# Optimization experiments

Measured on AMD Instinct MI355X. Metric: run time of the kernel, lower is better.

The kernel has to match this reference:

```python
import jax, jax.numpy as jnp
import numpy as np

LN_EPS = 1e-5  # torch.nn.LayerNorm default

def g(x):
    # minGRU activation: x + 0.5 for x >= 0, sigmoid(x) otherwise (always positive)
    return jnp.where(x >= 0, x + 0.5, jax.nn.sigmoid(x))

def log_g(x):
    return jnp.where(x >= 0, jnp.log(jax.nn.relu(x) + 0.5), -jax.nn.softplus(-x))

def layernorm(x, gamma, beta):
    mu = jnp.mean(x, axis=-1, keepdims=True)
    var = jnp.var(x, axis=-1, keepdims=True)
    return (x - mu) * jax.lax.rsqrt(var + LN_EPS) * gamma + beta

def mingru_scan(gate, hidden, h0):
    # gate, hidden: (B,S,D); h0: (B,1,D) positive
    # z = sigmoid(gate); h_t = (1-z_t)*h_{t-1} + z_t * g(hidden_t)
    # evaluated via Heinsen parallel scan in log space
    log_z = -jax.nn.softplus(-gate)          # log sigmoid(gate)
    log_coeffs = -jax.nn.softplus(gate)      # log(1 - sigmoid(gate))
    log_h0 = jnp.log(h0)                     # (B,1,D)
    log_tilde_h = log_g(hidden)
    a_star = jnp.cumsum(
        jnp.concatenate([jnp.zeros_like(log_h0), log_coeffs], axis=1), axis=1
    )                                        # (B,S+1,D)
    log_vals = jnp.concatenate([log_h0, log_z + log_tilde_h], axis=1) - a_star
    log_h = a_star + jax.lax.cumlogsumexp(log_vals, axis=1)
    return jnp.exp(log_h)[:, 1:]             # (B,S,D)

def setup_inputs() -> dict:
    key = jax.random.key(0)
    k1, k2 = jax.random.split(key)
    B, S, D, L = 8, 4096, 1024, 3
    x = jax.random.normal(k1, (B, S, D), dtype=jnp.float32)
    W = jax.random.normal(k2, (L, D, 2 * D), dtype=jnp.float32) * 0.02
    b = jnp.zeros((L, 2 * D), dtype=jnp.float32)
    ln_gamma = jnp.ones((L, D), dtype=jnp.float32)
    ln_beta = jnp.zeros((L, D), dtype=jnp.float32)
    return {"x": x, "ln_gamma": ln_gamma, "ln_beta": ln_beta, "W": W, "b": b}

def reference(x, ln_gamma, ln_beta, W, b):
    B, S, D = x.shape
    L = W.shape[0]
    inp = x
    next_hidden = []
    for l in range(L):
        h_prev = jnp.full((B, 1, D), 0.5, dtype=x.dtype)  # g(zeros) = 0.5
        xn = layernorm(inp, ln_gamma[l], ln_beta[l])
        gh = jnp.einsum('bsd,de->bse', xn, W[l]) + b[l]   # (B,S,2D)
        gate, hidden = jnp.split(gh, 2, axis=2)
        out = mingru_scan(gate, hidden, h_prev)
        next_hidden.append(out[:, -1:])
        out = out + inp  # residual (sizes equal -> identity res_align)
        inp = out
    return (out, *next_hidden)
```

## Files before the change

### kernel.cpp

```cpp
#include <hip/hip_runtime.h>

typedef unsigned short u16;
typedef unsigned int   u32;
typedef float  f32x4  __attribute__((ext_vector_type(4)));
typedef short  bf16x8 __attribute__((ext_vector_type(8)));
typedef u16    u16x4  __attribute__((ext_vector_type(4)));

#define BQ 8
#define SQ 4096
#define DQ 1024
#define NQ 2048
#define MQ 32768
#define KQ 1024
#define CCH 64
#define TCH 64
#define NT 16

__device__ __forceinline__ float bf2f(u16 u){
  union { u32 i; float f; } v; v.i = ((u32)u) << 16; return v.f;
}
__device__ __forceinline__ u16 f2bf(float f){
  union { float f; u32 i; } v; v.f = f;
  u32 r = v.i + 0x7fffu + ((v.i >> 16) & 1u);
  return (u16)(r >> 16);
}

__device__ __forceinline__ void sig_ab(float gate, float hid, float& a, float& bv){
  float eg = __expf(gate);
  float a_ = __builtin_amdgcn_rcpf(1.f + eg);
  float z  = 1.f - a_;
  float eh = __expf(hid);
  float sg = eh * __builtin_amdgcn_rcpf(1.f + eh);
  float gval = (hid >= 0.f) ? (hid + 0.5f) : sg;
  a = a_; bv = z * gval;
}

__device__ __forceinline__ void gload_lds16(const u16* g, u16* l){
  __builtin_amdgcn_global_load_lds(
      (const __attribute__((address_space(1))) u32*)g,
      (__attribute__((address_space(3)))       u32*)l,
      16, 0, 0);
}

__global__ __launch_bounds__(256) void wt_cast(const float* __restrict__ W,
                                               u16* __restrict__ WT){
  __shared__ float t[64][65];
  const int l  = blockIdx.z;
  const int k0 = blockIdx.x << 6, n0 = blockIdx.y << 6;
  const float* Wl = W  + (size_t)l * KQ * NQ;
  u16*         Tl = WT + (size_t)l * NQ * KQ;
  const int c = threadIdx.x & 63, r4 = threadIdx.x >> 6;
  #pragma unroll
  for (int i = 0; i < 16; ++i){
    int r = i * 4 + r4;
    t[r][c] = Wl[(size_t)(k0 + r) * NQ + n0 + c];
  }
  __syncthreads();
  #pragma unroll
  for (int i = 0; i < 16; ++i){
    int r = i * 4 + r4;
    Tl[(size_t)(n0 + r) * KQ + k0 + c] = f2bf(t[c][r]);
  }
}

__global__ __launch_bounds__(256) void ln_cast(const float* __restrict__ x,
                                               const float* __restrict__ gamma,
                                               const float* __restrict__ beta,
                                               u16* __restrict__ xn){
  const size_t row = blockIdx.x;
  const int tid = threadIdx.x;
  f32x4 xv = *(const f32x4*)(x + row * DQ + tid * 4);
  float s  = xv[0] + xv[1] + xv[2] + xv[3];
  float s2 = xv[0]*xv[0] + xv[1]*xv[1] + xv[2]*xv[2] + xv[3]*xv[3];
  #pragma unroll
  for (int off = 32; off > 0; off >>= 1){
    s  += __shfl_down(s,  off);
    s2 += __shfl_down(s2, off);
  }
  __shared__ float red[8];
  const int wave = tid >> 6, lane = tid & 63;
  if (lane == 0){ red[wave] = s; red[4 + wave] = s2; }
  __syncthreads();
  s  = red[0] + red[1] + red[2] + red[3];
  s2 = red[4] + red[5] + red[6] + red[7];
  const float mean = s * (1.f / DQ);
  float var = fmaxf(s2 * (1.f / DQ) - mean * mean, 0.f);
  const float rstd = rsqrtf(var + 1e-5f);
  f32x4 gv = *(const f32x4*)(gamma + tid * 4);
  f32x4 bv = *(const f32x4*)(beta  + tid * 4);
  u16x4 o;
  #pragma unroll
  for (int e = 0; e < 4; ++e) o[e] = f2bf((xv[e] - mean) * rstd * gv[e] + bv[e]);
  *(u16x4*)(xn + row * DQ + tid * 4) = o;
}

__global__ __launch_bounds__(512, 2) void gemm_k8(const u16* __restrict__ A,
                                                  const u16* __restrict__ Bt,
                                                  const float* __restrict__ bias,
                                                  u16* __restrict__ Cg){
  __shared__ u16 lds[2][2][2][8192];
  const int bid = blockIdx.x;
  const int swz = ((bid & 7) << 7) | (bid >> 3);
  const int bn = swz & 7, bm = swz >> 3;
  const int n0 = bn << 8, m0 = bm << 8;
  const int tid = threadIdx.x;
  const int w = tid >> 6, lane = tid & 63;
  const int wr = w >> 2, wc = w & 3;
  const int lr = lane & 15, hi = lane >> 4;
  const int sl8 = lane >> 3;
  const int sslot = (lane & 7) ^ sl8;

  f32x4 acc[2][2][4][2] = {};
  bf16x8 afr[4][2];
  bf16x8 bf0[2][2], bf1[2][2];

#define FENCE asm volatile("" ::: "memory")
#define BAR do { FENCE; __builtin_amdgcn_s_barrier(); FENCE; } while(0)

#define STAGE(op, hf, kt, pb_) do {                                             \
    const u16* gsrc_ = (op) ? Bt : A;                                           \
    const int rb_ = ((op) ? n0 : m0) + ((hf) << 7);                             \
    _Pragma("unroll")                                                           \
    for (int g_ = 0; g_ < 2; ++g_){                                             \
      const int row_ = (w << 4) + (g_ << 3) + sl8;                              \
      gload_lds16(gsrc_ + (size_t)(rb_ + row_) * KQ + ((kt) << 6) + (sslot << 3),\
                  &lds[pb_][op][hf][((w << 4) + (g_ << 3)) << 6]);              \
    }                                                                           \
  } while(0)

#define LDSRD(dst, base_, row_, slot_) do {                                     \
    const int r_ = (row_);                                                      \
    dst = *(const bf16x8*)((const char*)(base_) +                               \
          ((r_ << 7) + ((((slot_)) ^ (r_ & 7)) << 4)));                         \
  } while(0)

#define RD_A(hf) do {                                                           \
    const u16* Ah_ = &lds[pb][0][hf][0];                                        \
    _Pragma("unroll")                                                           \
    for (int i_ = 0; i_ < 4; ++i_)                                              \
      _Pragma("unroll")                                                         \
      for (int kk_ = 0; kk_ < 2; ++kk_)                                         \
        LDSRD(afr[i_][kk_], Ah_, (wr << 6) + (i_ << 4) + lr, (kk_ << 2) + hi);  \
  } while(0)

#define RD_B(dst, hf) do {                                                      \
    const u16* Bh_ = &lds[pb][1][hf][0];                                        \
    _Pragma("unroll")                                                           \
    for (int j_ = 0; j_ < 2; ++j_)                                              \
      _Pragma("unroll")                                                         \
      for (int kk_ = 0; kk_ < 2; ++kk_)                                         \
        LDSRD(dst[j_][kk_], Bh_, (wc << 5) + (j_ << 4) + lr, (kk_ << 2) + hi);  \
  } while(0)

#define MM(qm, qn, B) do {                                                      \
    _Pragma("unroll")                                                           \
    for (int i_ = 0; i_ < 4; ++i_)                                              \
      _Pragma("unroll")                                                         \
      for (int j_ = 0; j_ < 2; ++j_)                                            \
        _Pragma("unroll")                                                       \
        for (int kk_ = 0; kk_ < 2; ++kk_)                                       \
          acc[qm][qn][i_][j_] = __builtin_amdgcn_mfma_f32_16x16x32_bf16(        \
              afr[i_][kk_], B[j_][kk_], acc[qm][qn][i_][j_], 0, 0, 0);          \
  } while(0)

#define PH(VMW, STG, RDS, MFMAS) do {                                           \
    VMW;                                                                        \
    BAR;                                                                        \
    STG;                                                                        \
    RDS;                                                                        \
    asm volatile("s_waitcnt lgkmcnt(0)" ::: "memory");                          \
    __builtin_amdgcn_s_setprio(1);                                              \
    MFMAS;                                                                      \
    __builtin_amdgcn_s_setprio(0);                                              \
  } while(0)

  STAGE(1, 0, 0, 0); STAGE(0, 0, 0, 0); STAGE(1, 1, 0, 0); STAGE(0, 1, 0, 0);

  for (int t = 0; t < NT; ++t){
    const int pb = t & 1, qb = pb ^ 1;
    const bool s = (t + 1 < NT);
    PH(asm volatile("s_waitcnt vmcnt(4)" ::: "memory"),
       if (s) STAGE(1, 0, t + 1, qb),
       RD_A(0); RD_B(bf0, 0),
       MM(0, 0, bf0));
    PH(if (s) { asm volatile("s_waitcnt vmcnt(4)" ::: "memory"); }
       else   { asm volatile("s_waitcnt vmcnt(2)" ::: "memory"); },
       if (s) STAGE(0, 0, t + 1, qb),
       RD_B(bf1, 1),
       MM(0, 1, bf1));
    PH(if (s) { asm volatile("s_waitcnt vmcnt(4)" ::: "memory"); }
       else   { asm volatile("s_waitcnt vmcnt(0)" ::: "memory"); },
       if (s) STAGE(1, 1, t + 1, qb),
       RD_A(1),
       MM(1, 0, bf0));
    PH(,
       if (s) STAGE(0, 1, t + 1, qb),
       ,
       MM(1, 1, bf1));
  }
#undef PH
#undef MM
#undef RD_B
#undef RD_A
#undef LDSRD
#undef STAGE

  #pragma unroll
  for (int qn = 0; qn < 2; ++qn)
    #pragma unroll
    for (int j = 0; j < 2; ++j){
      const int col = n0 + (qn << 7) + (wc << 5) + (j << 4) + lr;
      const float bj = bias[col];
      #pragma unroll
      for (int qm = 0; qm < 2; ++qm)
        #pragma unroll
        for (int i = 0; i < 4; ++i){
          const int row0 = m0 + (qm << 7) + (wr << 6) + (i << 4) + (hi << 2);
          #pragma unroll
          for (int r = 0; r < 4; ++r)
            Cg[(size_t)(row0 + r) * NQ + col] = f2bf(acc[qm][qn][i][j][r] + bj);
        }
    }
#undef BAR
#undef FENCE
}

__global__ __launch_bounds__(256) void scan1(const u16* __restrict__ gh,
                                             float* __restrict__ P,
                                             float* __restrict__ Q){
  const int b = blockIdx.x >> 6;
  const int c = blockIdx.x & 63;
  const int d4 = threadIdx.x << 2;
  const u16* base = gh + ((size_t)(b * SQ + c * TCH) * NQ) + d4;
  float p[4] = {1.f,1.f,1.f,1.f}, q[4] = {0.f,0.f,0.f,0.f};
  for (int t = 0; t < TCH; ++t){
    u16x4 gv = *(const u16x4*)(base + (size_t)t * NQ);
    u16x4 hv = *(const u16x4*)(base + (size_t)t * NQ + DQ);
    #pragma unroll
    for (int e = 0; e < 4; ++e){
      float a, bv; sig_ab(bf2f(gv[e]), bf2f(hv[e]), a, bv);
      p[e] *= a; q[e] = a * q[e] + bv;
    }
  }
  const size_t o = ((size_t)blockIdx.x << 10) + d4;
  *(f32x4*)(P + o) = f32x4{p[0], p[1], p[2], p[3]};
  *(f32x4*)(Q + o) = f32x4{q[0], q[1], q[2], q[3]};
}

__global__ __launch_bounds__(256) void scan2(const float* __restrict__ P,
                                             const float* __restrict__ Q,
                                             float* __restrict__ hst,
                                             float* __restrict__ hlast){
  const int idx = blockIdx.x * 256 + threadIdx.x;
  const int b = idx >> 10, d = idx & 1023;
  float h = 0.5f;
  for (int c = 0; c < CCH; ++c){
    const size_t o = ((size_t)(b * CCH + c) << 10) + d;
    hst[o] = h;
    h = P[o] * h + Q[o];
  }
  hlast[idx] = h;
}

template<int MODE>
__global__ __launch_bounds__(256) void scan3f(const u16* __restrict__ gh,
                                              const float* __restrict__ hst,
                                              const void* __restrict__ inp,
                                              void* __restrict__ outp,
                                              u16* __restrict__ xn,
                                              const float* __restrict__ gamma,
                                              const float* __restrict__ beta){
  const int b = blockIdx.x >> 6;
  const int c = blockIdx.x & 63;
  const int tid = threadIdx.x;
  const int d4 = tid << 2;
  const int wave = tid >> 6, lane = tid & 63;
  const size_t srow = (size_t)(b * SQ + c * TCH);
  const u16* base = gh + srow * NQ + d4;
  const size_t o = ((size_t)blockIdx.x << 10) + d4;
  f32x4 h0v = *(const f32x4*)(hst + o);
  float h[4] = {h0v[0], h0v[1], h0v[2], h0v[3]};
  __shared__ float red[2][8];
  f32x4 gv = {}, bvv = {};
  if (MODE != 2){
    gv  = *(const f32x4*)(gamma + d4);
    bvv = *(const f32x4*)(beta  + d4);
  }
  for (int t = 0; t < TCH; ++t){
    u16x4 gg = *(const u16x4*)(base + (size_t)t * NQ);
    u16x4 hh = *(const u16x4*)(base + (size_t)t * NQ + DQ);
    f32x4 iv;
    if (MODE == 0){
      iv = *(const f32x4*)((const float*)inp + (srow + t) * DQ + d4);
    } else {
      u16x4 ib = *(const u16x4*)((const u16*)inp + (srow + t) * DQ + d4);
      #pragma unroll
      for (int e = 0; e < 4; ++e) iv[e] = bf2f(ib[e]);
    }
    f32x4 ov;
    #pragma unroll
    for (int e = 0; e < 4; ++e){
      float a, bv; sig_ab(bf2f(gg[e]), bf2f(hh[e]), a, bv);
      h[e] = a * h[e] + bv;
      ov[e] = h[e] + iv[e];
    }
    if (MODE == 2){
      *(f32x4*)((float*)outp + (srow + t) * DQ + d4) = ov;
    } else {
      u16x4 ob;
      #pragma unroll
      for (int e = 0; e < 4; ++e) ob[e] = f2bf(ov[e]);
      *(u16x4*)((u16*)outp + (srow + t) * DQ + d4) = ob;
      float s  = ov[0] + ov[1] + ov[2] + ov[3];
      float s2 = ov[0]*ov[0] + ov[1]*ov[1] + ov[2]*ov[2] + ov[3]*ov[3];
      #pragma unroll
      for (int off = 32; off > 0; off >>= 1){
        s  += __shfl_down(s,  off);
        s2 += __shfl_down(s2, off);
      }
      const int rb = t & 1;
      if (lane == 0){ red[rb][wave] = s; red[rb][4 + wave] = s2; }
      __syncthreads();
      s  = red[rb][0] + red[rb][1] + red[rb][2] + red[rb][3];
      s2 = red[rb][4] + red[rb][5] + red[rb][6] + red[rb][7];
      const float mean = s * (1.f / DQ);
      float var = fmaxf(s2 * (1.f / DQ) - mean * mean, 0.f);
      const float rstd = rsqrtf(var + 1e-5f);
      u16x4 xo;
      #pragma unroll
      for (int e = 0; e < 4; ++e)
        xo[e] = f2bf((ov[e] - mean) * rstd * gv[e] + bvv[e]);
      *(u16x4*)(xn + (srow + t) * DQ + d4) = xo;
    }
  }
}

extern "C" void kernel_launch(void* const* d_in, const int* in_sizes, int n_in,
                              void* d_out, int out_size, void* d_ws, size_t ws_size,
                              hipStream_t stream) {
  const float* x     = (const float*)d_in[0];
  const float* gamma = (const float*)d_in[1];
  const float* beta  = (const float*)d_in[2];
  const float* W     = (const float*)d_in[3];
  const float* bias  = (const float*)d_in[4];
  float* out = (float*)d_out;

  char* ws = (char*)d_ws;
  const size_t ACT = (size_t)MQ * DQ * 4;
  u16*   bufA = (u16*)(ws);
  u16*   bufB = (u16*)(ws + ACT);
  u16*   gh   = (u16*)  (ws + 2 * ACT);
  u16*   xn   = (u16*)  (ws + 3 * ACT);
  u16*   WT   = (u16*)  (ws + 3 * ACT + (size_t)MQ * DQ * 2);
  float* Pa   = (float*)(ws + 3 * ACT + (size_t)MQ * DQ * 2 + (size_t)3 * NQ * KQ * 2);
  float* Qa   = Pa + (size_t)BQ * CCH * DQ;
  float* hst  = Qa + (size_t)BQ * CCH * DQ;

  wt_cast<<<dim3(KQ / 64, NQ / 64, 3), 256, 0, stream>>>(W, WT);

  ln_cast<<<MQ, 256, 0, stream>>>(x, gamma, beta, xn);
  gemm_k8<<<dim3((NQ / 256) * (MQ / 256)), 512, 0, stream>>>(xn, WT, bias, gh);
  scan1<<<BQ * CCH, 256, 0, stream>>>(gh, Pa, Qa);
  scan2<<<(BQ * DQ) / 256, 256, 0, stream>>>(Pa, Qa, hst, out + (size_t)MQ * DQ);
  scan3f<0><<<BQ * CCH, 256, 0, stream>>>(gh, hst, x, bufA, xn,
                                          gamma + DQ, beta + DQ);
  gemm_k8<<<dim3((NQ / 256) * (MQ / 256)), 512, 0, stream>>>(
      xn, WT + (size_t)NQ * KQ, bias + NQ, gh);
  scan1<<<BQ * CCH, 256, 0, stream>>>(gh, Pa, Qa);
  scan2<<<(BQ * DQ) / 256, 256, 0, stream>>>(Pa, Qa, hst,
                                             out + (size_t)MQ * DQ + BQ * DQ);
  scan3f<1><<<BQ * CCH, 256, 0, stream>>>(gh, hst, bufA, bufB, xn,
                                          gamma + 2 * DQ, beta + 2 * DQ);
  gemm_k8<<<dim3((NQ / 256) * (MQ / 256)), 512, 0, stream>>>(
      xn, WT + (size_t)2 * NQ * KQ, bias + 2 * NQ, gh);
  scan1<<<BQ * CCH, 256, 0, stream>>>(gh, Pa, Qa);
  scan2<<<(BQ * DQ) / 256, 256, 0, stream>>>(Pa, Qa, hst,
                                             out + (size_t)MQ * DQ + 2 * BQ * DQ);
  scan3f<2><<<BQ * CCH, 256, 0, stream>>>(gh, hst, bufB, out, nullptr,
                                          nullptr, nullptr);
}
```

Measured before the change: 814.5 us.

## Fuse sigmoid coefficients and chunk scan summaries into the GEMM epilogue

The GEMM tiling changes so each block's N tile holds matching gate and hidden columns (128 of each). The epilogue then computes the recurrence coefficients a and b, stores them packed as bf16 pairs, and reduces per-64-row chunk (P,Q) summaries with cross-lane shuffles. This removes the scan1 kernel and its full re-read of the gate/hidden tensor, and scan3f no longer recomputes the sigmoids. The cost is a heavier GEMM epilogue with scattered 4-byte stores and a changed (P,Q) layout.

```diff
diff --git a/kernel.cpp b/kernel.cpp
--- a/kernel.cpp
+++ b/kernel.cpp
@@ -2,9 +2,11 @@
 
 typedef unsigned short u16;
 typedef unsigned int   u32;
+typedef float  f32x2  __attribute__((ext_vector_type(2)));
 typedef float  f32x4  __attribute__((ext_vector_type(4)));
 typedef short  bf16x8 __attribute__((ext_vector_type(8)));
 typedef u16    u16x4  __attribute__((ext_vector_type(4)));
+typedef u32    u32x4  __attribute__((ext_vector_type(4)));
 
 #define BQ 8
 #define SQ 4096
@@ -97,12 +99,13 @@
 __global__ __launch_bounds__(512, 2) void gemm_k8(const u16* __restrict__ A,
                                                   const u16* __restrict__ Bt,
                                                   const float* __restrict__ bias,
-                                                  u16* __restrict__ Cg){
+                                                  u32* __restrict__ abv,
+                                                  float* __restrict__ pq){
   __shared__ u16 lds[2][2][2][8192];
   const int bid = blockIdx.x;
   const int swz = ((bid & 7) << 7) | (bid >> 3);
   const int bn = swz & 7, bm = swz >> 3;
-  const int n0 = bn << 8, m0 = bm << 8;
+  const int m0 = bm << 8;
   const int tid = threadIdx.x;
   const int w = tid >> 6, lane = tid & 63;
   const int wr = w >> 2, wc = w & 3;
@@ -117,61 +120,61 @@
 #define FENCE asm volatile("" ::: "memory")
 #define BAR do { FENCE; __builtin_amdgcn_s_barrier(); FENCE; } while(0)
 
-#define STAGE(op, hf, kt, pb_) do {                                             \
-    const u16* gsrc_ = (op) ? Bt : A;                                           \
-    const int rb_ = ((op) ? n0 : m0) + ((hf) << 7);                             \
-    _Pragma("unroll")                                                           \
-    for (int g_ = 0; g_ < 2; ++g_){                                             \
-      const int row_ = (w << 4) + (g_ << 3) + sl8;                              \
+#define STAGE(op, hf, kt, pb_) do {                                            \
+    const u16* gsrc_ = (op) ? Bt : A;                                          \
+    const int rb_ = (op) ? ((bn << 7) + (hf) * 1024) : (m0 + ((hf) << 7));     \
+    _Pragma("unroll")                                                          \
+    for (int g_ = 0; g_ < 2; ++g_){                                            \
+      const int row_ = (w << 4) + (g_ << 3) + sl8;                             \
       gload_lds16(gsrc_ + (size_t)(rb_ + row_) * KQ + ((kt) << 6) + (sslot << 3),\
-                  &lds[pb_][op][hf][((w << 4) + (g_ << 3)) << 6]);              \
-    }                                                                           \
-  } while(0)
-
-#define LDSRD(dst, base_, row_, slot_) do {                                     \
-    const int r_ = (row_);                                                      \
-    dst = *(const bf16x8*)((const char*)(base_) +                               \
-          ((r_ << 7) + ((((slot_)) ^ (r_ & 7)) << 4)));                         \
-  } while(0)
-
-#define RD_A(hf) do {                                                           \
-    const u16* Ah_ = &lds[pb][0][hf][0];                                        \
-    _Pragma("unroll")                                                           \
-    for (int i_ = 0; i_ < 4; ++i_)                                              \
-      _Pragma("unroll")                                                         \
-      for (int kk_ = 0; kk_ < 2; ++kk_)                                         \
-        LDSRD(afr[i_][kk_], Ah_, (wr << 6) + (i_ << 4) + lr, (kk_ << 2) + hi);  \
-  } while(0)
-
-#define RD_B(dst, hf) do {                                                      \
-    const u16* Bh_ = &lds[pb][1][hf][0];                                        \
-    _Pragma("unroll")                                                           \
-    for (int j_ = 0; j_ < 2; ++j_)                                              \
-      _Pragma("unroll")                                                         \
-      for (int kk_ = 0; kk_ < 2; ++kk_)                                         \
-        LDSRD(dst[j_][kk_], Bh_, (wc << 5) + (j_ << 4) + lr, (kk_ << 2) + hi);  \
-  } while(0)
-
-#define MM(qm, qn, B) do {                                                      \
-    _Pragma("unroll")                                                           \
-    for (int i_ = 0; i_ < 4; ++i_)                                              \
-      _Pragma("unroll")                                                         \
-      for (int j_ = 0; j_ < 2; ++j_)                                            \
-        _Pragma("unroll")                                                       \
-        for (int kk_ = 0; kk_ < 2; ++kk_)                                       \
-          acc[qm][qn][i_][j_] = __builtin_amdgcn_mfma_f32_16x16x32_bf16(        \
-              afr[i_][kk_], B[j_][kk_], acc[qm][qn][i_][j_], 0, 0, 0);          \
-  } while(0)
-
-#define PH(VMW, STG, RDS, MFMAS) do {                                           \
-    VMW;                                                                        \
-    BAR;                                                                        \
-    STG;                                                                        \
-    RDS;                                                                        \
-    asm volatile("s_waitcnt lgkmcnt(0)" ::: "memory");                          \
-    __builtin_amdgcn_s_setprio(1);                                              \
-    MFMAS;                                                                      \
-    __builtin_amdgcn_s_setprio(0);                                              \
+                  &lds[pb_][op][hf][((w << 4) + (g_ << 3)) << 6]);             \
+    }                                                                          \
+  } while(0)
+
+#define LDSRD(dst, base_, row_, slot_) do {                                    \
+    const int r_ = (row_);                                                     \
+    dst = *(const bf16x8*)((const char*)(base_) +                              \
+          ((r_ << 7) + ((((slot_)) ^ (r_ & 7)) << 4)));                        \
+  } while(0)
+
+#define RD_A(hf) do {                                                          \
+    const u16* Ah_ = &lds[pb][0][hf][0];                                       \
+    _Pragma("unroll")                                                          \
+    for (int i_ = 0; i_ < 4; ++i_)                                             \
+      _Pragma("unroll")                                                        \
+      for (int kk_ = 0; kk_ < 2; ++kk_)                                        \
+        LDSRD(afr[i_][kk_], Ah_, (wr << 6) + (i_ << 4) + lr, (kk_ << 2) + hi); \
+  } while(0)
+
+#define RD_B(dst, hf) do {                                                     \
+    const u16* Bh_ = &lds[pb][1][hf][0];                                       \
+    _Pragma("unroll")                                                          \
+    for (int j_ = 0; j_ < 2; ++j_)                                             \
+      _Pragma("unroll")                                                        \
+      for (int kk_ = 0; kk_ < 2; ++kk_)                                        \
+        LDSRD(dst[j_][kk_], Bh_, (wc << 5) + (j_ << 4) + lr, (kk_ << 2) + hi); \
+  } while(0)
+
+#define MM(qm, qn, B) do {                                                     \
+    _Pragma("unroll")                                                          \
+    for (int i_ = 0; i_ < 4; ++i_)                                             \
+      _Pragma("unroll")                                                        \
+      for (int j_ = 0; j_ < 2; ++j_)                                           \
+        _Pragma("unroll")                                                      \
+        for (int kk_ = 0; kk_ < 2; ++kk_)                                      \
+          acc[qm][qn][i_][j_] = __builtin_amdgcn_mfma_f32_16x16x32_bf16(       \
+              afr[i_][kk_], B[j_][kk_], acc[qm][qn][i_][j_], 0, 0, 0);         \
+  } while(0)
+
+#define PH(VMW, STG, RDS, MFMAS) do {                                          \
+    VMW;                                                                       \
+    BAR;                                                                       \
+    STG;                                                                       \
+    RDS;                                                                       \
+    asm volatile("s_waitcnt lgkmcnt(0)" ::: "memory");                         \
+    __builtin_amdgcn_s_setprio(1);                                             \
+    MFMAS;                                                                     \
+    __builtin_amdgcn_s_setprio(0);                                             \
   } while(0)
 
   STAGE(1, 0, 0, 0); STAGE(0, 0, 0, 0); STAGE(1, 1, 0, 0); STAGE(0, 1, 0, 0);
@@ -205,50 +208,56 @@
 #undef LDSRD
 #undef STAGE
 
-  #pragma unroll
-  for (int qn = 0; qn < 2; ++qn)
+  const int dbase = (bn << 7) + (wc << 5) + lr;
+  #pragma unroll
+  for (int qm = 0; qm < 2; ++qm){
+    const int row00 = m0 + (qm << 7) + (wr << 6);
+    float chP[2] = {1.f, 1.f}, chQ[2] = {0.f, 0.f};
     #pragma unroll
-    for (int j = 0; j < 2; ++j){
-      const int col = n0 + (qn << 7) + (wc << 5) + (j << 4) + lr;
-      const float bj = bias[col];
-      #pragma unroll
-      for (int qm = 0; qm < 2; ++qm)
+    for (int i = 0; i < 4; ++i){
+      float sgP[2] = {1.f, 1.f}, sgQ[2] = {0.f, 0.f};
+      #pragma unroll
+      for (int r = 0; r < 4; ++r){
+        const int row = row00 + (i << 4) + (hi << 2) + r;
         #pragma unroll
-        for (int i = 0; i < 4; ++i){
-          const int row0 = m0 + (qm << 7) + (wr << 6) + (i << 4) + (hi << 2);
-          #pragma unroll
-          for (int r = 0; r < 4; ++r)
-            Cg[(size_t)(row0 + r) * NQ + col] = f2bf(acc[qm][qn][i][j][r] + bj);
+        for (int j = 0; j < 2; ++j){
+          const int d = dbase + (j << 4);
+          float gate = acc[qm][0][i][j][r] + bias[d];
+          float hid  = acc[qm][1][i][j][r] + bias[1024 + d];
+          float a, bv; sig_ab(gate, hid, a, bv);
+          const u16 ua = f2bf(a), ub = f2bf(bv);
+          abv[(size_t)row * 1024 + d] = (u32)ua | ((u32)ub << 16);
+          const float ar = bf2f(ua), br = bf2f(ub);
+          sgQ[j] = ar * sgQ[j] + br;
+          sgP[j] *= ar;
         }
-    }
+      }
+      #pragma unroll
+      for (int j = 0; j < 2; ++j){
+        float p = sgP[j], q = sgQ[j];
+        float p1 = __shfl_up(p, 16), q1 = __shfl_up(q, 16);
+        if (hi >= 1){ q = p * q1 + q; p = p * p1; }
+        float p2 = __shfl_up(p, 32), q2 = __shfl_up(q, 32);
+        if (hi >= 2){ q = p * q2 + q; p = p * p2; }
+        chQ[j] = p * chQ[j] + q;
+        chP[j] = p * chP[j];
+      }
+    }
+    if (hi == 3){
+      const int bq = row00 >> 12, cq = (row00 >> 6) & 63;
+      #pragma unroll
+      for (int j = 0; j < 2; ++j){
+        const int d = dbase + (j << 4);
+        f32x2 v; v[0] = chP[j]; v[1] = chQ[j];
+        *(f32x2*)(pq + ((((size_t)(bq * CCH + cq)) << 10) + d) * 2) = v;
+      }
+    }
+  }
 #undef BAR
 #undef FENCE
 }
 
-__global__ __launch_bounds__(256) void scan1(const u16* __restrict__ gh,
-                                             float* __restrict__ P,
-                                             float* __restrict__ Q){
-  const int b = blockIdx.x >> 6;
-  const int c = blockIdx.x & 63;
-  const int d4 = threadIdx.x << 2;
-  const u16* base = gh + ((size_t)(b * SQ + c * TCH) * NQ) + d4;
-  float p[4] = {1.f,1.f,1.f,1.f}, q[4] = {0.f,0.f,0.f,0.f};
-  for (int t = 0; t < TCH; ++t){
-    u16x4 gv = *(const u16x4*)(base + (size_t)t * NQ);
-    u16x4 hv = *(const u16x4*)(base + (size_t)t * NQ + DQ);
-    #pragma unroll
-    for (int e = 0; e < 4; ++e){
-      float a, bv; sig_ab(bf2f(gv[e]), bf2f(hv[e]), a, bv);
-      p[e] *= a; q[e] = a * q[e] + bv;
-    }
-  }
-  const size_t o = ((size_t)blockIdx.x << 10) + d4;
-  *(f32x4*)(P + o) = f32x4{p[0], p[1], p[2], p[3]};
-  *(f32x4*)(Q + o) = f32x4{q[0], q[1], q[2], q[3]};
-}
-
-__global__ __launch_bounds__(256) void scan2(const float* __restrict__ P,
-                                             const float* __restrict__ Q,
+__global__ __launch_bounds__(256) void scan2(const float* __restrict__ pq,
                                              float* __restrict__ hst,
                                              float* __restrict__ hlast){
   const int idx = blockIdx.x * 256 + threadIdx.x;
@@ -257,13 +266,14 @@
   for (int c = 0; c < CCH; ++c){
     const size_t o = ((size_t)(b * CCH + c) << 10) + d;
     hst[o] = h;
-    h = P[o] * h + Q[o];
+    f32x2 v = *(const f32x2*)(pq + o * 2);
+    h = v[0] * h + v[1];
   }
   hlast[idx] = h;
 }
 
 template<int MODE>
-__global__ __launch_bounds__(256) void scan3f(const u16* __restrict__ gh,
+__global__ __launch_bounds__(256) void scan3f(const u32* __restrict__ abv,
                                               const float* __restrict__ hst,
                                               const void* __restrict__ inp,
                                               void* __restrict__ outp,
@@ -276,7 +286,7 @@
   const int d4 = tid << 2;
   const int wave = tid >> 6, lane = tid & 63;
   const size_t srow = (size_t)(b * SQ + c * TCH);
-  const u16* base = gh + srow * NQ + d4;
+  const u32* base = abv + srow * 1024 + d4;
   const size_t o = ((size_t)blockIdx.x << 10) + d4;
   f32x4 h0v = *(const f32x4*)(hst + o);
   float h[4] = {h0v[0], h0v[1], h0v[2], h0v[3]};
@@ -287,8 +297,7 @@
     bvv = *(const f32x4*)(beta  + d4);
   }
   for (int t = 0; t < TCH; ++t){
-    u16x4 gg = *(const u16x4*)(base + (size_t)t * NQ);
-    u16x4 hh = *(const u16x4*)(base + (size_t)t * NQ + DQ);
+    u32x4 ab = *(const u32x4*)(base + (size_t)t * 1024);
     f32x4 iv;
     if (MODE == 0){
       iv = *(const f32x4*)((const float*)inp + (srow + t) * DQ + d4);
@@ -300,7 +309,8 @@
     f32x4 ov;
     #pragma unroll
     for (int e = 0; e < 4; ++e){
-      float a, bv; sig_ab(bf2f(gg[e]), bf2f(hh[e]), a, bv);
+      const float a  = bf2f((u16)(ab[e] & 0xffffu));
+      const float bv = bf2f((u16)(ab[e] >> 16));
       h[e] = a * h[e] + bv;
       ov[e] = h[e] + iv[e];
     }
@@ -349,33 +359,30 @@
   const size_t ACT = (size_t)MQ * DQ * 4;
   u16*   bufA = (u16*)(ws);
   u16*   bufB = (u16*)(ws + ACT);
-  u16*   gh   = (u16*)  (ws + 2 * ACT);
-  u16*   xn   = (u16*)  (ws + 3 * ACT);
-  u16*   WT   = (u16*)  (ws + 3 * ACT + (size_t)MQ * DQ * 2);
-  float* Pa   = (float*)(ws + 3 * ACT + (size_t)MQ * DQ * 2 + (size_t)3 * NQ * KQ * 2);
-  float* Qa   = Pa + (size_t)BQ * CCH * DQ;
-  float* hst  = Qa + (size_t)BQ * CCH * DQ;
+  u32*   abv  = (u32*)(ws + 2 * ACT);
+  u16*   xn   = (u16*)(ws + 3 * ACT);
+  u16*   WT   = (u16*)(ws + 3 * ACT + (size_t)MQ * DQ * 2);
+  float* pq   = (float*)(ws + 3 * ACT + (size_t)MQ * DQ * 2 + (size_t)3 * NQ * KQ * 2);
+  float* hst  = pq + (size_t)2 * BQ * CCH * DQ;
 
   wt_cast<<<dim3(KQ / 64, NQ / 64, 3), 256, 0, stream>>>(W, WT);
 
+  const dim3 ggrid((NQ / 256) * (MQ / 256));
   ln_cast<<<MQ, 256, 0, stream>>>(x, gamma, beta, xn);
-  gemm_k8<<<dim3((NQ / 256) * (MQ / 256)), 512, 0, stream>>>(xn, WT, bias, gh);
-  scan1<<<BQ * CCH, 256, 0, stream>>>(gh, Pa, Qa);
-  scan2<<<(BQ * DQ) / 256, 256, 0, stream>>>(Pa, Qa, hst, out + (size_t)MQ * DQ);
-  scan3f<0><<<BQ * CCH, 256, 0, stream>>>(gh, hst, x, bufA, xn,
+  gemm_k8<<<ggrid, 512, 0, stream>>>(xn, WT, bias, abv, pq);
+  scan2<<<(BQ * DQ) / 256, 256, 0, stream>>>(pq, hst, out + (size_t)MQ * DQ);
+  scan3f<0><<<BQ * CCH, 256, 0, stream>>>(abv, hst, x, bufA, xn,
                                           gamma + DQ, beta + DQ);
-  gemm_k8<<<dim3((NQ / 256) * (MQ / 256)), 512, 0, stream>>>(
-      xn, WT + (size_t)NQ * KQ, bias + NQ, gh);
-  scan1<<<BQ * CCH, 256, 0, stream>>>(gh, Pa, Qa);
-  scan2<<<(BQ * DQ) / 256, 256, 0, stream>>>(Pa, Qa, hst,
+  gemm_k8<<<ggrid, 512, 0, stream>>>(xn, WT + (size_t)NQ * KQ, bias + NQ,
+                                     abv, pq);
+  scan2<<<(BQ * DQ) / 256, 256, 0, stream>>>(pq, hst,
                                              out + (size_t)MQ * DQ + BQ * DQ);
-  scan3f<1><<<BQ * CCH, 256, 0, stream>>>(gh, hst, bufA, bufB, xn,
+  scan3f<1><<<BQ * CCH, 256, 0, stream>>>(abv, hst, bufA, bufB, xn,
                                           gamma + 2 * DQ, beta + 2 * DQ);
-  gemm_k8<<<dim3((NQ / 256) * (MQ / 256)), 512, 0, stream>>>(
-      xn, WT + (size_t)2 * NQ * KQ, bias + 2 * NQ, gh);
-  scan1<<<BQ * CCH, 256, 0, stream>>>(gh, Pa, Qa);
-  scan2<<<(BQ * DQ) / 256, 256, 0, stream>>>(Pa, Qa, hst,
+  gemm_k8<<<ggrid, 512, 0, stream>>>(xn, WT + (size_t)2 * NQ * KQ, bias + 2 * NQ,
+                                     abv, pq);
+  scan2<<<(BQ * DQ) / 256, 256, 0, stream>>>(pq, hst,
                                              out + (size_t)MQ * DQ + 2 * BQ * DQ);
-  scan3f<2><<<BQ * CCH, 256, 0, stream>>>(gh, hst, bufB, out, nullptr,
+  scan3f<2><<<BQ * CCH, 256, 0, stream>>>(abv, hst, bufB, out, nullptr,
                                           nullptr, nullptr);
 }
```

Measured after the change: 732.5 us. 10.1% less time.
